# Performance work log

Hardware: AMD Instinct MI355X
Metric: run time of the kernel (lower is better)

## Reference

```python
import jax, jax.numpy as jnp
import numpy as np

B, D, L = 8, 512, 4096
NHEAD = 8
HEAD_DIM = D // NHEAD
TRUNC_STD = 0.02


def setup_inputs() -> dict:
    key = jax.random.key(0)
    ks = jax.random.split(key, 7)
    return {
        "x": jax.random.normal(ks[0], (B, D, L, 1), jnp.float32),
        "y": jax.random.normal(ks[1], (B, D, 1, 1), jnp.float32),
        "Wq": jax.random.normal(ks[2], (D, D), jnp.float32) * TRUNC_STD,
        "Wk": jax.random.normal(ks[3], (D, D), jnp.float32) * TRUNC_STD,
        "Wv": jax.random.normal(ks[4], (D, D), jnp.float32) * TRUNC_STD,
        "WO_ring": jax.random.normal(ks[5], (D, D), jnp.float32) * TRUNC_STD,
        "bO_ring": jnp.zeros((D,), jnp.float32),
        "WO_star": jax.random.normal(ks[6], (D, D), jnp.float32) * TRUNC_STD,
        "bO_star": jnp.zeros((D,), jnp.float32),
    }


def reference(x, y, Wq, Wk, Wv, WO_ring, bO_ring, WO_star, bO_star):
    Bx, Dx, Lx, _ = x.shape
    hd = Dx // NHEAD
    scale = 1.0 / np.sqrt(hd).astype(np.float32)

    # concat relay token on the sequence axis, project q/k/v over channels
    xy = jnp.concatenate([x, y], axis=2)[..., 0]            # [B, D, L+1]
    xy = jnp.transpose(xy, (0, 2, 1))                       # [B, L+1, D]
    q = jnp.transpose(xy @ Wq, (0, 2, 1))                   # [B, D, L+1]
    k = jnp.transpose(xy @ Wk, (0, 2, 1))
    v = jnp.transpose(xy @ Wv, (0, 2, 1))

    # ---- ring (local window-3 + relay) attention over the L node tokens ----
    qn = q[:, :, :Lx].reshape(Bx, NHEAD, hd, Lx)            # [B,n,h,L]
    kn, vn = k[:, :, :Lx], v[:, :, :Lx]                     # [B,D,L]
    kr, vr = k[:, :, Lx], v[:, :, Lx]                       # [B,D]

    def window3(t):
        # extract_patches SAME with size 3: slot w holds t[:, :, l-1+w], zero-padded
        tp = jnp.pad(t, ((0, 0), (0, 0), (1, 1)))
        tw = jnp.stack([tp[:, :, w:w + Lx] for w in range(3)], axis=2)  # [B,D,3,L]
        return tw.reshape(Bx, NHEAD, hd, 3, Lx)

    kr_b = jnp.broadcast_to(kr.reshape(Bx, NHEAD, hd, 1, 1), (Bx, NHEAD, hd, 1, Lx))
    vr_b = jnp.broadcast_to(vr.reshape(Bx, NHEAD, hd, 1, 1), (Bx, NHEAD, hd, 1, Lx))
    kw = jnp.concatenate([window3(kn), kr_b], axis=3)       # [B,n,h,4,L]
    vw = jnp.concatenate([window3(vn), vr_b], axis=3)

    scores = jnp.einsum('bnhl,bnhwl->bnwl', qn, kw) * scale  # [B,n,4,L]
    alphas = jax.nn.softmax(scores, axis=2)                  # softmax over window
    att = jnp.einsum('bnwl,bnhwl->bnhl', alphas, vw).reshape(Bx, Dx, Lx)
    nodes = jnp.einsum('bdl,de->bel', att, WO_ring) + bO_ring[None, :, None]
    nodes = nodes[..., None]                                 # [B, D, L, 1]

    # ---- star (relay) attention: relay query attends to all L+1 tokens ----
    qr = q[:, :, Lx].reshape(Bx, NHEAD, 1, hd)              # [B,n,1,h]
    ka = k.reshape(Bx, NHEAD, hd, Lx + 1)                   # [B,n,h,L+1]
    va = v.reshape(Bx, NHEAD, hd, Lx + 1)
    s = jnp.einsum('bnoh,bnhl->bnol', qr, ka) * scale       # [B,n,1,L+1]
    a = jax.nn.softmax(s, axis=-1)
    att_r = jnp.einsum('bnol,bnhl->bnoh', a, va).reshape(Bx, Dx)
    relay = (att_r @ WO_star + bO_star).reshape(Bx, Dx, 1, 1)

    return nodes, relay
```

## Files before the change

### kernel.cpp

```cpp
#include <hip/hip_runtime.h>

#define BB 8
#define DD 512
#define LL 4096
#define NH 8
#define HD 64
#define SCALE 0.125f
#define NCH 16
#define CH 256

typedef __attribute__((ext_vector_type(8))) short short8;
typedef __attribute__((ext_vector_type(4))) float f32x4;

static __device__ __forceinline__ float bf2f(unsigned short u) {
  union { float f; unsigned int i; } c; c.i = ((unsigned int)u) << 16; return c.f;
}
static __device__ __forceinline__ unsigned short f2bf(float f) {
  union { float f; unsigned int i; } c; c.f = f;
  unsigned int i = c.i;
  unsigned int r = (i + 0x7fffu + ((i >> 16) & 1u)) >> 16;
  return (unsigned short)r;
}

static __device__ __forceinline__ void gload_lds16(const void* g, void* l) {
  __builtin_amdgcn_global_load_lds(
      (const __attribute__((address_space(1))) void*)g,
      (__attribute__((address_space(3))) void*)l, 16, 0, 0);
}

static __device__ __forceinline__ float waveSum(float v) {
#pragma unroll
  for (int o = 32; o; o >>= 1) v += __shfl_down(v, o, 64);
  return v;
}
static __device__ __forceinline__ float waveMax(float v) {
#pragma unroll
  for (int o = 32; o; o >>= 1) v = fmaxf(v, __shfl_down(v, o, 64));
  return v;
}
static __device__ __forceinline__ float grp8Sum(float v) {
  v += __shfl_xor(v, 1, 8);
  v += __shfl_xor(v, 2, 8);
  v += __shfl_xor(v, 4, 8);
  return v;
}
static __device__ float blockSum(float v, float* red) {
  const int lane = threadIdx.x & 63, wid = threadIdx.x >> 6;
  const int nw = (int)(blockDim.x >> 6);
  v = waveSum(v);
  if (lane == 0) red[wid] = v;
  __syncthreads();
  if (wid == 0) {
    float t = (lane < nw) ? red[lane] : 0.f;
    t = waveSum(t);
    if (lane == 0) red[0] = t;
  }
  __syncthreads();
  float r = red[0];
  __syncthreads();
  return r;
}
static __device__ float blockMax(float v, float* red) {
  const int lane = threadIdx.x & 63, wid = threadIdx.x >> 6;
  const int nw = (int)(blockDim.x >> 6);
  v = waveMax(v);
  if (lane == 0) red[wid] = v;
  __syncthreads();
  if (wid == 0) {
    float t = (lane < nw) ? red[lane] : -1e30f;
    t = waveMax(t);
    if (lane == 0) red[0] = t;
  }
  __syncthreads();
  float r = red[0];
  __syncthreads();
  return r;
}

__global__ __launch_bounds__(256) void prep_w(
    const float* __restrict__ win, unsigned short* __restrict__ wout) {
  const int d0 = blockIdx.y * 64;
  const int m0 = blockIdx.x * 64;
  __shared__ float t[64][65];
  const int tid = threadIdx.x;
  const int r = tid >> 4;
  const int c4 = (tid & 15) * 4;
#pragma unroll
  for (int p = 0; p < 4; p++) {
    const float4 v = *(const float4*)(win + (size_t)(d0 + p * 16 + r) * DD + m0 + c4);
    *(float4*)&t[p * 16 + r][c4] = v;
  }
  __syncthreads();
#pragma unroll
  for (int p = 0; p < 4; p++) {
    const int ll = p * 16 + r;
    ushort4 o;
    o.x = f2bf(t[c4 + 0][ll]);
    o.y = f2bf(t[c4 + 1][ll]);
    o.z = f2bf(t[c4 + 2][ll]);
    o.w = f2bf(t[c4 + 3][ll]);
    *(ushort4*)(wout + (size_t)(m0 + ll) * DD + d0 + c4) = o;
  }
}

__global__ __launch_bounds__(256) void prep_x(
    const float* __restrict__ x, unsigned short* __restrict__ xt) {
  const int b = blockIdx.z;
  const int e0 = blockIdx.y * 64;
  const int l0 = blockIdx.x * 64;
  __shared__ float t[64][65];
  const int tid = threadIdx.x;
  const int r = tid >> 4;
  const int c4 = (tid & 15) * 4;
  const float* xb = x + (size_t)b * DD * LL;
#pragma unroll
  for (int p = 0; p < 4; p++) {
    const float4 v = *(const float4*)(xb + (size_t)(e0 + p * 16 + r) * LL + l0 + c4);
    *(float4*)&t[p * 16 + r][c4] = v;
  }
  __syncthreads();
#pragma unroll
  for (int p = 0; p < 4; p++) {
    const int ll = p * 16 + r;
    ushort4 o;
    o.x = f2bf(t[c4 + 0][ll]);
    o.y = f2bf(t[c4 + 1][ll]);
    o.z = f2bf(t[c4 + 2][ll]);
    o.w = f2bf(t[c4 + 3][ll]);
    *(ushort4*)(xt + ((size_t)b * LL + l0 + ll) * DD + e0 + c4) = o;
  }
}

__global__ __launch_bounds__(256) void qkv_mfma(
    const unsigned short* __restrict__ Wt, const unsigned short* __restrict__ Xt,
    unsigned short* __restrict__ qn, unsigned short* __restrict__ kn,
    unsigned short* __restrict__ vn) {
  const int b = blockIdx.z;
  const int m0 = blockIdx.y * 128;
  const int n0 = blockIdx.x * 128;
  __shared__ __align__(16) unsigned short smem[128 * 136];
  short* As = (short*)smem;
  short* Bs = (short*)(smem + 128 * 32);
  const int tid = threadIdx.x;
  const int lane = tid & 63, w = tid >> 6;
  const int wm = w & 1, wn = w >> 1;

  const unsigned short* Ag = Wt + (size_t)m0 * DD;
  const unsigned short* Bg = Xt + ((size_t)b * LL + n0) * DD;
  const int srow = lane >> 2;
  const int scol = (lane & 3) * 8;

  f32x4 acc[4][4];
#pragma unroll
  for (int i = 0; i < 4; i++)
#pragma unroll
    for (int j = 0; j < 4; j++) acc[i][j] = (f32x4){0.f, 0.f, 0.f, 0.f};

  for (int k0 = 0; k0 < DD; k0 += 32) {
    __syncthreads();
#pragma unroll
    for (int p = 0; p < 2; p++) {
      const int c = w * 2 + p;
      gload_lds16(Ag + (size_t)(c * 16 + srow) * DD + k0 + scol, As + c * 16 * 32);
      gload_lds16(Bg + (size_t)(c * 16 + srow) * DD + k0 + scol, Bs + c * 16 * 32);
    }
    __syncthreads();
    short8 af[4], bfr[4];
#pragma unroll
    for (int i = 0; i < 4; i++)
      af[i] = *(const short8*)&As[(wm * 64 + i * 16 + (lane & 15)) * 32 + (lane >> 4) * 8];
#pragma unroll
    for (int j = 0; j < 4; j++)
      bfr[j] = *(const short8*)&Bs[(wn * 64 + j * 16 + (lane & 15)) * 32 + (lane >> 4) * 8];
#pragma unroll
    for (int i = 0; i < 4; i++)
#pragma unroll
      for (int j = 0; j < 4; j++)
        acc[i][j] = __builtin_amdgcn_mfma_f32_16x16x32_bf16(af[i], bfr[j], acc[i][j], 0, 0, 0);
  }

  __syncthreads();
  const int lb = wn * 64 + (lane & 15);
  const int db = wm * 64 + ((lane >> 4) << 2);
#pragma unroll
  for (int i = 0; i < 4; i++)
#pragma unroll
    for (int j = 0; j < 4; j++) {
      ushort4 pk;
      pk.x = f2bf(acc[i][j][0]); pk.y = f2bf(acc[i][j][1]);
      pk.z = f2bf(acc[i][j][2]); pk.w = f2bf(acc[i][j][3]);
      *(ushort4*)&smem[(lb + j * 16) * 136 + db + i * 16] = pk;
    }
  __syncthreads();
  const int sector = m0 >> 9;
  unsigned short* outp = ((sector == 0) ? qn : ((sector == 1) ? kn : vn)) + (size_t)b * LL * DD;
  const int d0 = m0 & 511;
#pragma unroll
  for (int it = 0; it < 8; it++) {
    const int flat = it * 2048 + tid * 8;
    const int row = flat >> 7;
    const int col = flat & 127;
    const short8 vdat = *(const short8*)&smem[row * 136 + col];
    *(short8*)(outp + (size_t)(n0 + row) * DD + d0 + col) = vdat;
  }
}

__global__ __launch_bounds__(256) void nodes_mfma(
    const unsigned short* __restrict__ Wt, const unsigned short* __restrict__ At,
    const float* __restrict__ bo, float* __restrict__ out) {
  const int b = blockIdx.z;
  const int m0 = blockIdx.y * 128;
  const int n0 = blockIdx.x * 128;
  __shared__ short As[128 * 32];
  __shared__ short Bs[128 * 32];
  const int tid = threadIdx.x;
  const int lane = tid & 63, w = tid >> 6;
  const int wm = w & 1, wn = w >> 1;

  const unsigned short* Ag = Wt + (size_t)m0 * DD;
  const unsigned short* Bg = At + ((size_t)b * LL + n0) * DD;
  const int srow = lane >> 2;
  const int scol = (lane & 3) * 8;

  f32x4 acc[4][4];
#pragma unroll
  for (int i = 0; i < 4; i++)
#pragma unroll
    for (int j = 0; j < 4; j++) acc[i][j] = (f32x4){0.f, 0.f, 0.f, 0.f};

  for (int k0 = 0; k0 < DD; k0 += 32) {
    __syncthreads();
#pragma unroll
    for (int p = 0; p < 2; p++) {
      const int c = w * 2 + p;
      gload_lds16(Ag + (size_t)(c * 16 + srow) * DD + k0 + scol, (short*)As + c * 16 * 32);
      gload_lds16(Bg + (size_t)(c * 16 + srow) * DD + k0 + scol, (short*)Bs + c * 16 * 32);
    }
    __syncthreads();
    short8 af[4], bfr[4];
#pragma unroll
    for (int i = 0; i < 4; i++)
      af[i] = *(const short8*)&As[(wm * 64 + i * 16 + (lane & 15)) * 32 + (lane >> 4) * 8];
#pragma unroll
    for (int j = 0; j < 4; j++)
      bfr[j] = *(const short8*)&Bs[(wn * 64 + j * 16 + (lane & 15)) * 32 + (lane >> 4) * 8];
#pragma unroll
    for (int i = 0; i < 4; i++)
#pragma unroll
      for (int j = 0; j < 4; j++)
        acc[i][j] = __builtin_amdgcn_mfma_f32_16x16x32_bf16(af[i], bfr[j], acc[i][j], 0, 0, 0);
  }

  float* outp = out + (size_t)b * DD * LL;
  const int ebase = m0 + wm * 64;
  const int col0 = n0 + wn * 64 + (lane & 15);
#pragma unroll
  for (int i = 0; i < 4; i++) {
    const int e0 = ebase + i * 16 + (lane >> 4) * 4;
#pragma unroll
    for (int j = 0; j < 4; j++) {
      const int cc = col0 + j * 16;
#pragma unroll
      for (int r = 0; r < 4; r++)
        outp[(size_t)(e0 + r) * LL + cc] = acc[i][j][r] + bo[e0 + r];
    }
  }
}

__global__ __launch_bounds__(256) void relay_qkv(
    const float* __restrict__ y, const float* __restrict__ Wq,
    const float* __restrict__ Wk, const float* __restrict__ Wv,
    float* __restrict__ qr, float* __restrict__ kr, float* __restrict__ vr) {
  const int b = blockIdx.y;
  const int d = blockIdx.x * 256 + threadIdx.x;
  __shared__ float ys[DD];
  for (int i = threadIdx.x; i < DD; i += 256) ys[i] = y[b * DD + i];
  __syncthreads();
  float aq = 0.f, ak = 0.f, av = 0.f;
  for (int e = 0; e < DD; e++) {
    const float yv = ys[e];
    aq = fmaf(yv, Wq[(size_t)e * DD + d], aq);
    ak = fmaf(yv, Wk[(size_t)e * DD + d], ak);
    av = fmaf(yv, Wv[(size_t)e * DD + d], av);
  }
  qr[b * DD + d] = aq;
  kr[b * DD + d] = ak;
  vr[b * DD + d] = av;
}

__global__ __launch_bounds__(256) void local_attn(
    const unsigned short* __restrict__ qn, const unsigned short* __restrict__ kn,
    const unsigned short* __restrict__ vn, const float* __restrict__ kr,
    const float* __restrict__ vr, unsigned short* __restrict__ att_t) {
  const int b = blockIdx.z, n = blockIdx.y;
  const int tid = threadIdx.x;
  const int li = tid >> 3, dl = tid & 7;
  const int l = blockIdx.x * 32 + li;
  __shared__ float krs[HD], vrs[HD];
  const int rb = b * DD + n * HD;
  if (tid < HD) { krs[tid] = kr[rb + tid]; vrs[tid] = vr[rb + tid]; }
  __syncthreads();

  const size_t rowbase = ((size_t)b * LL + l) * DD + n * HD + dl * 8;
  const unsigned short* qp = qn + rowbase;
  const unsigned short* kp = kn + rowbase;
  const unsigned short* vp = vn + rowbase;
  const bool has_m = (l > 0), has_p = (l < LL - 1);
  const long moff = has_m ? -(long)DD : 0;
  const long poff = has_p ? (long)DD : 0;

  const short8 q8 = *(const short8*)qp;
  const short8 km8 = *(const short8*)(kp + moff);
  const short8 k08 = *(const short8*)kp;
  const short8 kp8 = *(const short8*)(kp + poff);

  float s0 = 0.f, s1 = 0.f, s2 = 0.f, s3 = 0.f;
  float qf[8];
#pragma unroll
  for (int j = 0; j < 8; j++) {
    qf[j] = bf2f((unsigned short)q8[j]);
    s0 = fmaf(qf[j], bf2f((unsigned short)km8[j]), s0);
    s1 = fmaf(qf[j], bf2f((unsigned short)k08[j]), s1);
    s2 = fmaf(qf[j], bf2f((unsigned short)kp8[j]), s2);
    s3 = fmaf(qf[j], krs[dl * 8 + j], s3);
  }
  s0 = grp8Sum(s0) * SCALE;
  s1 = grp8Sum(s1) * SCALE;
  s2 = grp8Sum(s2) * SCALE;
  s3 = grp8Sum(s3) * SCALE;
  if (!has_m) s0 = 0.f;
  if (!has_p) s2 = 0.f;
  const float m = fmaxf(fmaxf(s0, s1), fmaxf(s2, s3));
  const float e0 = __expf(s0 - m), e1 = __expf(s1 - m);
  const float e2 = __expf(s2 - m), e3 = __expf(s3 - m);
  const float inv = 1.f / (e0 + e1 + e2 + e3);
  const float a0 = has_m ? e0 * inv : 0.f;
  const float a1 = e1 * inv;
  const float a2 = has_p ? e2 * inv : 0.f;
  const float a3 = e3 * inv;

  const short8 vm8 = *(const short8*)(vp + moff);
  const short8 v08 = *(const short8*)vp;
  const short8 vp8 = *(const short8*)(vp + poff);
  short8 o8;
#pragma unroll
  for (int j = 0; j < 8; j++) {
    float o = a0 * bf2f((unsigned short)vm8[j]) + a1 * bf2f((unsigned short)v08[j]) +
              a2 * bf2f((unsigned short)vp8[j]) + a3 * vrs[dl * 8 + j];
    o8[j] = (short)f2bf(o);
  }
  *(short8*)(att_t + rowbase) = o8;
}

__global__ __launch_bounds__(256) void relay_attn_part(
    const float* __restrict__ qr, const unsigned short* __restrict__ kn,
    const unsigned short* __restrict__ vn, float* __restrict__ part) {
  const int ch = blockIdx.x, n = blockIdx.y, b = blockIdx.z;
  const int tid = threadIdx.x;
  const int li = tid >> 3, dl = tid & 7;
  __shared__ float qs[HD];
  __shared__ float sv[CH];
  __shared__ float red[17];
  __shared__ float os[32][68];
  const int rb = b * DD + n * HD;
  if (tid < HD) qs[tid] = qr[rb + tid];
  __syncthreads();
  const size_t base = ((size_t)b * LL + ch * CH) * DD + n * HD + dl * 8;

#pragma unroll
  for (int it = 0; it < 8; it++) {
    const int lr2 = it * 32 + li;
    const short8 kc = *(const short8*)(kn + base + (size_t)lr2 * DD);
    float p = 0.f;
#pragma unroll
    for (int j = 0; j < 8; j++) p = fmaf(qs[dl * 8 + j], bf2f((unsigned short)kc[j]), p);
    p = grp8Sum(p);
    if (dl == 0) sv[lr2] = p * SCALE;
  }
  __syncthreads();
  const float s = sv[tid];
  const float m = blockMax(s, red);
  const float pp = __expf(s - m);
  sv[tid] = pp;
  const float sum = blockSum(pp, red);

  float oc[8];
#pragma unroll
  for (int j = 0; j < 8; j++) oc[j] = 0.f;
#pragma unroll
  for (int it = 0; it < 8; it++) {
    const int lr2 = it * 32 + li;
    const float p = sv[lr2];
    const short8 vc = *(const short8*)(vn + base + (size_t)lr2 * DD);
#pragma unroll
    for (int j = 0; j < 8; j++) oc[j] = fmaf(p, bf2f((unsigned short)vc[j]), oc[j]);
  }
#pragma unroll
  for (int j = 0; j < 8; j++) os[li][dl * 8 + j] = oc[j];
  __syncthreads();
  float* po = part + (((size_t)b * NH + n) * NCH + ch) * 68;
  if (tid < HD) {
    float t = 0.f;
#pragma unroll 8
    for (int g = 0; g < 32; g++) t += os[g][tid];
    po[tid] = t;
  }
  if (tid == 64) { po[64] = m; po[65] = sum; }
}

__global__ __launch_bounds__(64) void relay_attn_combine(
    const float* __restrict__ qr, const float* __restrict__ krr,
    const float* __restrict__ vrr, const float* __restrict__ part,
    float* __restrict__ attr) {
  const int n = blockIdx.x, b = blockIdx.y;
  const int h = threadIdx.x;
  const int rb = b * DD + n * HD;
  float t = qr[rb + h] * krr[rb + h];
  t = waveSum(t);
  const float s_r = __shfl(t, 0, 64) * SCALE;
  const float* po = part + (((size_t)b * NH + n) * NCH) * 68;
  float M = s_r;
#pragma unroll
  for (int c = 0; c < NCH; c++) M = fmaxf(M, po[c * 68 + 64]);
  float S = __expf(s_r - M);
  float o = S * vrr[rb + h];
#pragma unroll
  for (int c = 0; c < NCH; c++) {
    const float e = __expf(po[c * 68 + 64] - M);
    S = fmaf(po[c * 68 + 65], e, S);
    o = fmaf(po[c * 68 + h], e, o);
  }
  attr[rb + h] = o / S;
}

__global__ __launch_bounds__(256) void relay_proj(
    const float* __restrict__ attr, const float* __restrict__ Wstar,
    const float* __restrict__ bstar, float* __restrict__ out) {
  const int b = blockIdx.y;
  const int e = blockIdx.x * 256 + threadIdx.x;
  __shared__ float as[DD];
  for (int i = threadIdx.x; i < DD; i += 256) as[i] = attr[b * DD + i];
  __syncthreads();
  float acc = bstar[e];
  for (int d = 0; d < DD; d++) acc = fmaf(as[d], Wstar[(size_t)d * DD + e], acc);
  out[(size_t)BB * DD * LL + b * DD + e] = acc;
}

extern "C" void kernel_launch(void* const* d_in, const int* in_sizes, int n_in,
                              void* d_out, int out_size, void* d_ws, size_t ws_size,
                              hipStream_t stream) {
  const float* x   = (const float*)d_in[0];
  const float* y   = (const float*)d_in[1];
  const float* Wq  = (const float*)d_in[2];
  const float* Wk  = (const float*)d_in[3];
  const float* Wv  = (const float*)d_in[4];
  const float* WOr = (const float*)d_in[5];
  const float* bOr = (const float*)d_in[6];
  const float* WOs = (const float*)d_in[7];
  const float* bOs = (const float*)d_in[8];
  float* out = (float*)d_out;

  char* ws = (char*)d_ws;
  const size_t SZ = (size_t)BB * DD * LL * sizeof(unsigned short);
  unsigned short* qn  = (unsigned short*)(ws);
  unsigned short* kn  = (unsigned short*)(ws + SZ);
  unsigned short* vn  = (unsigned short*)(ws + 2 * SZ);
  unsigned short* xt  = (unsigned short*)(ws + 3 * SZ);
  unsigned short* att_t = xt;
  unsigned short* Wallt = (unsigned short*)(ws + 4 * SZ);
  unsigned short* WOrt  = (unsigned short*)(ws + 4 * SZ + 1536 * 512 * 2);
  float* qr   = (float*)(ws + 4 * SZ + 2048 * 512 * 2);
  float* kr   = qr + BB * DD;
  float* vr   = kr + BB * DD;
  float* attr = vr + BB * DD;
  float* part = attr + BB * DD;

  prep_w<<<dim3(8, 8), 256, 0, stream>>>(Wq, Wallt);
  prep_w<<<dim3(8, 8), 256, 0, stream>>>(Wk, Wallt + (size_t)512 * 512);
  prep_w<<<dim3(8, 8), 256, 0, stream>>>(Wv, Wallt + (size_t)1024 * 512);
  prep_w<<<dim3(8, 8), 256, 0, stream>>>(WOr, WOrt);
  prep_x<<<dim3(64, 8, BB), 256, 0, stream>>>(x, xt);

  qkv_mfma<<<dim3(32, 12, BB), 256, 0, stream>>>(Wallt, xt, qn, kn, vn);
  relay_qkv<<<dim3(DD / 256, BB), 256, 0, stream>>>(y, Wq, Wk, Wv, qr, kr, vr);
  local_attn<<<dim3(LL / 32, NH, BB), 256, 0, stream>>>(qn, kn, vn, kr, vr, att_t);
  nodes_mfma<<<dim3(32, 4, BB), 256, 0, stream>>>(WOrt, att_t, bOr, out);
  relay_attn_part<<<dim3(NCH, NH, BB), 256, 0, stream>>>(qr, kn, vn, part);
  relay_attn_combine<<<dim3(NH, BB), 64, 0, stream>>>(qr, kr, vr, part, attr);
  relay_proj<<<dim3(DD / 256, BB), 256, 0, stream>>>(attr, WOs, bOs, out);
}
```

Measured before the change: 323.3 us.

## Rewrite QKV GEMM as 256x256 tile, double-buffered, phase-scheduled MFMA kernel

```diff
diff --git a/kernel.cpp b/kernel.cpp
--- a/kernel.cpp
+++ b/kernel.cpp
@@ -131,77 +131,150 @@
   }
 }
 
-__global__ __launch_bounds__(256) void qkv_mfma(
+#define STAGEH(g, s)                                       \
+  do {                                                     \
+    gload_lds16((g) + sgoff, (s) + sloff);                 \
+    gload_lds16((g) + sgoff + 32, (s) + sloff + 4096);     \
+  } while (0)
+
+#define READ_A(dst, base, ib)                                           \
+  _Pragma("unroll") for (int i = 0; i < 4; i++) {                       \
+    dst[i][0] = *(const short8*)((base) + ((ib) + i) * 512);            \
+    dst[i][1] = *(const short8*)((base) + ((ib) + i) * 512 + 4096);     \
+  }
+
+#define READ_B(base, qn_)                                               \
+  _Pragma("unroll") for (int j = 0; j < 2; j++) {                       \
+    bb[j][0] = *(const short8*)((base) + (qn_) * 1024 + j * 512);       \
+    bb[j][1] = *(const short8*)((base) + (qn_) * 1024 + j * 512 + 4096);\
+  }
+
+#define MFMA16(AF, IO, JO)                                                    \
+  __builtin_amdgcn_s_setprio(1);                                              \
+  _Pragma("unroll") for (int i = 0; i < 4; i++)                               \
+  _Pragma("unroll") for (int j = 0; j < 2; j++) {                             \
+    acc[(IO) + i][(JO) + j] = __builtin_amdgcn_mfma_f32_16x16x32_bf16(        \
+        AF[i][0], bb[j][0], acc[(IO) + i][(JO) + j], 0, 0, 0);                \
+    acc[(IO) + i][(JO) + j] = __builtin_amdgcn_mfma_f32_16x16x32_bf16(        \
+        AF[i][1], bb[j][1], acc[(IO) + i][(JO) + j], 0, 0, 0);                \
+  }                                                                           \
+  __builtin_amdgcn_s_setprio(0);
+
+#define PHASE_SYNC_PRE                                     \
+  __builtin_amdgcn_s_barrier();                            \
+  asm volatile("s_waitcnt lgkmcnt(0)" ::: "memory");       \
+  __builtin_amdgcn_sched_barrier(0);
+
+#define PHASE_SYNC_POST                                    \
+  __builtin_amdgcn_sched_barrier(0);                       \
+  __builtin_amdgcn_s_barrier();
+
+__global__ __launch_bounds__(512, 2) void qkv_mfma_8ph(
     const unsigned short* __restrict__ Wt, const unsigned short* __restrict__ Xt,
     unsigned short* __restrict__ qn, unsigned short* __restrict__ kn,
     unsigned short* __restrict__ vn) {
+  extern __shared__ __align__(16) unsigned short sm[];
   const int b = blockIdx.z;
-  const int m0 = blockIdx.y * 128;
-  const int n0 = blockIdx.x * 128;
-  __shared__ __align__(16) unsigned short smem[128 * 136];
-  short* As = (short*)smem;
-  short* Bs = (short*)(smem + 128 * 32);
+  const int m0 = blockIdx.y * 256;
+  const int n0 = blockIdx.x * 256;
   const int tid = threadIdx.x;
   const int lane = tid & 63, w = tid >> 6;
-  const int wm = w & 1, wn = w >> 1;
+  const int wm = w >> 2, wn = w & 3;
+  const int l15 = lane & 15, lh = lane >> 4;
 
   const unsigned short* Ag = Wt + (size_t)m0 * DD;
   const unsigned short* Bg = Xt + ((size_t)b * LL + n0) * DD;
-  const int srow = lane >> 2;
-  const int scol = (lane & 3) * 8;
-
-  f32x4 acc[4][4];
-#pragma unroll
-  for (int i = 0; i < 4; i++)
+
+  const int kswz = (lh << 3) ^ ((l15 & 8) << 1);
+  const unsigned short* aB = sm + wm * 8192 + l15 * 32 + kswz;
+  const unsigned short* bB = sm + 32768 + (wn >> 1) * 8192 + (wn & 1) * 2048 +
+                             l15 * 32 + kswz;
+
+  const int srow = (w << 4) + (lane >> 2);
+  const size_t sgoff = (size_t)srow * DD + ((size_t)(((lane & 3) << 3) ^ ((srow & 8) << 1)));
+  const int sloff = w * 512;
+
+  f32x4 acc[8][4];
+#pragma unroll
+  for (int i = 0; i < 8; i++)
 #pragma unroll
     for (int j = 0; j < 4; j++) acc[i][j] = (f32x4){0.f, 0.f, 0.f, 0.f};
 
-  for (int k0 = 0; k0 < DD; k0 += 32) {
-    __syncthreads();
-#pragma unroll
-    for (int p = 0; p < 2; p++) {
-      const int c = w * 2 + p;
-      gload_lds16(Ag + (size_t)(c * 16 + srow) * DD + k0 + scol, As + c * 16 * 32);
-      gload_lds16(Bg + (size_t)(c * 16 + srow) * DD + k0 + scol, Bs + c * 16 * 32);
+  STAGEH(Ag, sm);
+  STAGEH(Ag + 128 * DD, sm + 8192);
+  STAGEH(Bg, sm + 32768);
+  STAGEH(Bg + 128 * DD, sm + 32768 + 8192);
+  STAGEH(Ag + 64, sm + 16384);
+  STAGEH(Ag + 128 * DD + 64, sm + 16384 + 8192);
+  asm volatile("s_waitcnt vmcnt(4)" ::: "memory");
+  __builtin_amdgcn_s_barrier();
+
+  short8 a0[4][2], a1[4][2], bb[2][2];
+  for (int u = 0; u < 8; ++u) {
+    const int slot = u & 1;
+    const unsigned short* aS = aB + slot * 16384;
+    const unsigned short* bS = bB + slot * 16384;
+    const unsigned short* An = Ag + (u + 2) * 64;
+    const unsigned short* Bn = Bg + (u + 1) * 64;
+    unsigned short* sAd = sm + slot * 16384;
+    unsigned short* sBd = sm + 32768 + (slot ^ 1) * 16384;
+
+    READ_A(a0, aS, 0);
+    READ_B(bS, 0);
+    if (u < 7) STAGEH(Bn, sBd);
+    PHASE_SYNC_PRE
+    MFMA16(a0, 0, 0)
+    PHASE_SYNC_POST
+    READ_A(a1, aS, 4);
+    if (u < 7) STAGEH(Bn + 128 * DD, sBd + 8192);
+    PHASE_SYNC_PRE
+    MFMA16(a1, 4, 0)
+    PHASE_SYNC_POST
+    READ_B(bS, 1);
+    if (u < 6) STAGEH(An, sAd);
+    PHASE_SYNC_PRE
+    MFMA16(a0, 0, 2)
+    PHASE_SYNC_POST
+    if (u < 6) STAGEH(An + 128 * DD, sAd + 8192);
+    __builtin_amdgcn_s_barrier();
+    asm volatile("s_waitcnt lgkmcnt(0)" ::: "memory");
+    __builtin_amdgcn_sched_barrier(0);
+    MFMA16(a1, 4, 2)
+    __builtin_amdgcn_sched_barrier(0);
+    if (u < 6) {
+      asm volatile("s_waitcnt vmcnt(4)" ::: "memory");
+    } else if (u == 6) {
+      asm volatile("s_waitcnt vmcnt(0)" ::: "memory");
     }
-    __syncthreads();
-    short8 af[4], bfr[4];
-#pragma unroll
-    for (int i = 0; i < 4; i++)
-      af[i] = *(const short8*)&As[(wm * 64 + i * 16 + (lane & 15)) * 32 + (lane >> 4) * 8];
-#pragma unroll
-    for (int j = 0; j < 4; j++)
-      bfr[j] = *(const short8*)&Bs[(wn * 64 + j * 16 + (lane & 15)) * 32 + (lane >> 4) * 8];
-#pragma unroll
-    for (int i = 0; i < 4; i++)
-#pragma unroll
-      for (int j = 0; j < 4; j++)
-        acc[i][j] = __builtin_amdgcn_mfma_f32_16x16x32_bf16(af[i], bfr[j], acc[i][j], 0, 0, 0);
-  }
-
-  __syncthreads();
-  const int lb = wn * 64 + (lane & 15);
-  const int db = wm * 64 + ((lane >> 4) << 2);
-#pragma unroll
-  for (int i = 0; i < 4; i++)
+    __builtin_amdgcn_s_barrier();
+  }
+
+  __syncthreads();
+#pragma unroll
+  for (int i = 0; i < 8; i++)
 #pragma unroll
     for (int j = 0; j < 4; j++) {
+      const int dloc = wm * 128 + i * 16 + lh * 4;
+      const int lloc = wn * 64 + j * 16 + l15;
       ushort4 pk;
-      pk.x = f2bf(acc[i][j][0]); pk.y = f2bf(acc[i][j][1]);
-      pk.z = f2bf(acc[i][j][2]); pk.w = f2bf(acc[i][j][3]);
-      *(ushort4*)&smem[(lb + j * 16) * 136 + db + i * 16] = pk;
+      pk.x = f2bf(acc[i][j][0]);
+      pk.y = f2bf(acc[i][j][1]);
+      pk.z = f2bf(acc[i][j][2]);
+      pk.w = f2bf(acc[i][j][3]);
+      *(ushort4*)((char*)sm + ((lloc * 512 + dloc * 2) ^ ((lloc & 7) << 4))) = pk;
     }
   __syncthreads();
   const int sector = m0 >> 9;
-  unsigned short* outp = ((sector == 0) ? qn : ((sector == 1) ? kn : vn)) + (size_t)b * LL * DD;
-  const int d0 = m0 & 511;
-#pragma unroll
-  for (int it = 0; it < 8; it++) {
-    const int flat = it * 2048 + tid * 8;
-    const int row = flat >> 7;
-    const int col = flat & 127;
-    const short8 vdat = *(const short8*)&smem[row * 136 + col];
-    *(short8*)(outp + (size_t)(n0 + row) * DD + d0 + col) = vdat;
+  unsigned short* outp = ((sector == 0) ? qn : (sector == 1) ? kn : vn) +
+                         (size_t)b * LL * DD + (m0 & 511);
+#pragma unroll
+  for (int it = 0; it < 16; it++) {
+    const int flat = it * 8192 + tid * 16;
+    const int lloc = flat >> 9;
+    const int off = flat & 511;
+    const short8 vdat =
+        *(const short8*)((const char*)sm + lloc * 512 + (off ^ ((lloc & 7) << 4)));
+    *(short8*)(outp + (size_t)(n0 + lloc) * DD + (off >> 1)) = vdat;
   }
 }
 
@@ -475,13 +548,20 @@
   float* attr = vr + BB * DD;
   float* part = attr + BB * DD;
 
+  static int smaxset = 0;
+  if (!smaxset) {
+    (void)hipFuncSetAttribute((const void*)qkv_mfma_8ph,
+                              hipFuncAttributeMaxDynamicSharedMemorySize, 131072);
+    smaxset = 1;
+  }
+
   prep_w<<<dim3(8, 8), 256, 0, stream>>>(Wq, Wallt);
   prep_w<<<dim3(8, 8), 256, 0, stream>>>(Wk, Wallt + (size_t)512 * 512);
   prep_w<<<dim3(8, 8), 256, 0, stream>>>(Wv, Wallt + (size_t)1024 * 512);
   prep_w<<<dim3(8, 8), 256, 0, stream>>>(WOr, WOrt);
   prep_x<<<dim3(64, 8, BB), 256, 0, stream>>>(x, xt);
 
-  qkv_mfma<<<dim3(32, 12, BB), 256, 0, stream>>>(Wallt, xt, qn, kn, vn);
+  qkv_mfma_8ph<<<dim3(16, 6, BB), 512, 131072, stream>>>(Wallt, xt, qn, kn, vn);
   relay_qkv<<<dim3(DD / 256, BB), 256, 0, stream>>>(y, Wq, Wk, Wv, qr, kr, vr);
   local_attn<<<dim3(LL / 32, NH, BB), 256, 0, stream>>>(qn, kn, vn, kr, vr, att_t);
   nodes_mfma<<<dim3(32, 4, BB), 256, 0, stream>>>(WOrt, att_t, bOr, out);
```

Result: faster. 316.0 us (-2.3%).
